# Performance work log

Measured on AMD Instinct MI355X. Metric: run time of the kernel, lower is better.

## Reference

```python
import jax, jax.numpy as jnp
import numpy as np

N = 50000          # num nodes
DEG = 16           # constant out-degree -> edges[:,0] sorted, every node present
E = N * DEG
NODE_IN = 128
NODE_OUT = 64
EDGE_IN = 128
EDGE_OUT = 64      # must equal NODE_OUT for the reshape in the original module


def _xavier_uniform(key, shape):
    fan_in, fan_out = shape[0], shape[1]
    a = np.sqrt(6.0 / (fan_in + fan_out)).astype(np.float32)
    return jax.random.uniform(key, shape, jnp.float32, -a, a)


def setup_inputs() -> dict:
    key = jax.random.key(0)
    k1, k2, k3, k4, k5, k6, k7 = jax.random.split(key, 7)
    node_fts = jax.random.normal(k1, (N, NODE_IN), jnp.float32)
    edge_fts = jax.random.normal(k2, (N, EDGE_IN), jnp.float32)
    # sorted sources with constant degree so unique(src).shape[0] == N and
    # the original's repeat(bincount) trick is equivalent to gather-by-src
    src = jnp.repeat(jnp.arange(N, dtype=jnp.int32), DEG)
    dst = jax.random.randint(k3, (E,), 0, N, dtype=jnp.int32)
    edges = jnp.stack([src, dst], axis=1)  # [E, 2]
    W_node = _xavier_uniform(k4, (NODE_IN, NODE_OUT))
    W_edge = _xavier_uniform(k5, (EDGE_IN, EDGE_OUT))
    a_node = _xavier_uniform(k6, (2 * NODE_OUT, 1))
    a_edge = _xavier_uniform(k7, (NODE_OUT + EDGE_OUT, 1))
    return {"node_fts": node_fts, "edge_fts": edge_fts, "edges": edges,
            "W_node": W_node, "W_edge": W_edge,
            "a_node": a_node, "a_edge": a_edge}


def reference(node_fts, edge_fts, edges, W_node, W_edge, a_node, a_edge):
    src = edges[:, 0]
    h_v = node_fts @ W_node            # [N, NODE_OUT]
    e_v = edge_fts @ W_edge            # [N, EDGE_OUT]

    # gather endpoint features -> [E, 2*NODE_OUT] / [E, NODE_OUT+EDGE_OUT]
    h_pair = h_v[edges].reshape(-1, 2 * NODE_OUT)
    e_pair = e_v[edges].reshape(-1, NODE_OUT + EDGE_OUT)

    leaky = lambda x: jnp.where(x > 0, x, 0.2 * x)
    node_att = leaky((h_pair @ a_node)[:, 0])   # [E]
    edge_att = leaky((e_pair @ a_edge)[:, 0])   # [E]

    node_att = jnp.exp(jnp.clip(node_att, -2.0, 2.0))
    edge_att = jnp.exp(jnp.clip(edge_att, -2.0, 2.0))

    node_sum = jax.ops.segment_sum(node_att, src, num_segments=N)
    edge_sum = jax.ops.segment_sum(edge_att, src, num_segments=N)

    node_att_norm = node_att / node_sum[src]
    edge_att_norm = edge_att / edge_sum[src]

    node_att_var = jnp.var(node_att_norm, ddof=1)  # torch.var is unbiased
    edge_att_var = jnp.var(edge_att_norm, ddof=1)

    node_out = jax.ops.segment_sum(h_pair * node_att_norm[:, None], src, num_segments=N)
    edge_out = jax.ops.segment_sum(e_pair * edge_att_norm[:, None], src, num_segments=N)
    return node_out, edge_out, node_att_var, edge_att_var
```

## Files before the change

### kernel.cpp

```cpp
#include <hip/hip_runtime.h>
#include <hip/hip_bf16.h>

#define NN 50000
#define DEG 16
#define EE (NN*DEG)
#define CHUNKS 3125

typedef unsigned int uint;
typedef unsigned short ushort;
typedef __attribute__((ext_vector_type(8))) short bf16x8;
typedef __attribute__((ext_vector_type(4))) float f32x4;

__device__ inline ushort f2b(float f){
  return __bfloat16_as_ushort(__float2bfloat16(f));
}
__device__ inline float b2f(uint lo16){ return __uint_as_float(lo16 << 16); }
__device__ inline float bhi(uint v){ return __uint_as_float(v & 0xffff0000u); }

__global__ __launch_bounds__(256) void prep_kernel(
    const float* __restrict__ W0, const float* __restrict__ W1,
    uint4* __restrict__ wf)
{
  const int pass = blockIdx.y;
  const float* W = pass ? W1 : W0;
  const int t    = threadIdx.x;
  const int f    = blockIdx.x*4 + (t >> 6);
  const int lane = t & 63;
  const int kt = f >> 2, nt = f & 3;
  const int n  = nt*16 + (lane & 15);
  const int k0 = kt*32 + (lane >> 4)*8;
  uint4 pk;
  ushort* ps = (ushort*)&pk;
  #pragma unroll
  for (int j = 0; j < 8; j++) ps[j] = f2b(W[(k0 + j)*64 + n]);
  wf[(pass*16 + f)*64 + lane] = pk;
}

__global__ __launch_bounds__(256) void gemm_mfma_kernel(
    const float* __restrict__ in0, const float* __restrict__ in1,
    const uint4* __restrict__ wf,
    const float* __restrict__ a0,  const float* __restrict__ a1,
    ushort* __restrict__ hev,
    float* __restrict__ s1ne, float* __restrict__ s2ne)
{
  const int pass = blockIdx.y;
  const float* in = pass ? in1 : in0;
  const float* av = pass ? a1  : a0;

  const int tid  = threadIdx.x;
  const int wv   = tid >> 6;
  const int lane = tid & 63;
  const int g    = lane >> 4;
  const int c    = lane & 15;

  const int ch = blockIdx.x*4 + wv;
  if (ch >= CHUNKS) return;
  const int r0 = ch * 16;

  bf16x8 wfrag[16];
  const uint4* wfp = wf + (long)pass*16*64 + lane;
  #pragma unroll
  for (int f = 0; f < 16; f++) {
    uint4 v = wfp[f*64];
    wfrag[f] = *(bf16x8*)&v;
  }
  float a1r[4][4], a2r[4][4];
  #pragma unroll
  for (int nt = 0; nt < 4; nt++)
    #pragma unroll
    for (int v = 0; v < 4; v++) {
      a1r[nt][v] = av[nt*16 + g*4 + v];
      a2r[nt][v] = av[64 + nt*16 + g*4 + v];
    }

  const float* rowp = in + (long)(r0 + c)*128 + g*8;
  float4 ald[8];
  #pragma unroll
  for (int kt = 0; kt < 4; kt++) {
    ald[kt*2]   = *(const float4*)(rowp + kt*32);
    ald[kt*2+1] = *(const float4*)(rowp + kt*32 + 4);
  }

  f32x4 acc[4];
  #pragma unroll
  for (int nt = 0; nt < 4; nt++) acc[nt] = (f32x4){0.f, 0.f, 0.f, 0.f};
  #pragma unroll
  for (int kt = 0; kt < 4; kt++) {
    const float4 u = ald[kt*2], w = ald[kt*2+1];
    bf16x8 af;
    af[0] = (short)f2b(u.x); af[1] = (short)f2b(u.y);
    af[2] = (short)f2b(u.z); af[3] = (short)f2b(u.w);
    af[4] = (short)f2b(w.x); af[5] = (short)f2b(w.y);
    af[6] = (short)f2b(w.z); af[7] = (short)f2b(w.w);
    #pragma unroll
    for (int nt = 0; nt < 4; nt++)
      acc[nt] = __builtin_amdgcn_mfma_f32_16x16x32_bf16(wfrag[kt*4+nt], af, acc[nt], 0, 0, 0);
  }

  float t1 = 0.f, t2 = 0.f;
  #pragma unroll
  for (int nt = 0; nt < 4; nt++)
    #pragma unroll
    for (int v = 0; v < 4; v++) {
      t1 = fmaf(acc[nt][v], a1r[nt][v], t1);
      t2 = fmaf(acc[nt][v], a2r[nt][v], t2);
    }
  t1 += __shfl_xor(t1, 16); t1 += __shfl_xor(t1, 32);
  t2 += __shfl_xor(t2, 16); t2 += __shfl_xor(t2, 32);
  if (lane < 16) {
    s1ne[(long)(r0 + lane)*2 + pass] = t1;
    s2ne[(long)(r0 + lane)*2 + pass] = t2;
  }

  ushort* rowt = hev + (long)(r0 + c)*128 + pass*64 + g*4;
  #pragma unroll
  for (int nt = 0; nt < 4; nt++) {
    uint2 pkv;
    pkv.x = (uint)f2b(acc[nt][0]) | ((uint)f2b(acc[nt][1]) << 16);
    pkv.y = (uint)f2b(acc[nt][2]) | ((uint)f2b(acc[nt][3]) << 16);
    *(uint2*)(rowt + nt*16) = pkv;
  }
}

__global__ __launch_bounds__(256) void attn_kernel(
    const uint* __restrict__ hev,
    const float2* __restrict__ s1ne, const float2* __restrict__ s2ne,
    const int* __restrict__ edges,
    float* __restrict__ outp, double* __restrict__ partials)
{
  const int tid  = threadIdx.x;
  const int wv   = tid >> 6;
  const int lane = tid & 63;
  const int j    = lane >> 4;
  const int cl   = lane & 15;
  double a_qn = 0.0, a_qe = 0.0;
  float* node_out = outp;
  float* edge_out = outp + (long)NN*128;
  const int NG = NN/4;

#define LOADT(dest, T) { \
    _Pragma("unroll") \
    for (int m = 0; m < 4; m++) { \
      const int sl = (T)*16 + m*4 + j; \
      const int d  = __shfl(dst, sl); \
      dest[m] = *(const uint4*)(hev + (long)d*64 + cl*4); \
    } }

#define COMB(T, src) { \
    float ac[8]; \
    _Pragma("unroll") for (int u = 0; u < 8; u++) ac[u] = 0.f; \
    _Pragma("unroll") \
    for (int m = 0; m < 4; m++) { \
      const int sl = (T)*16 + m*4 + j; \
      const float w2n = __shfl(wn, sl); \
      const float w2e = __shfl(we, sl); \
      const float wk  = (cl < 8) ? w2n : w2e; \
      const uint4 v = src[m]; \
      ac[0] = fmaf(wk, b2f(v.x & 0xffffu), ac[0]); \
      ac[1] = fmaf(wk, bhi(v.x),           ac[1]); \
      ac[2] = fmaf(wk, b2f(v.y & 0xffffu), ac[2]); \
      ac[3] = fmaf(wk, bhi(v.y),           ac[3]); \
      ac[4] = fmaf(wk, b2f(v.z & 0xffffu), ac[4]); \
      ac[5] = fmaf(wk, bhi(v.z),           ac[5]); \
      ac[6] = fmaf(wk, b2f(v.w & 0xffffu), ac[6]); \
      ac[7] = fmaf(wk, bhi(v.w),           ac[7]); \
    } \
    _Pragma("unroll") \
    for (int u = 0; u < 8; u++) { \
      ac[u] += __shfl_xor(ac[u], 16); \
      ac[u] += __shfl_xor(ac[u], 32); \
    } \
    if (lane < 16) { \
      float* base = ((cl < 8) ? node_out : edge_out) \
                    + (long)(i0 + (T))*128 + 64 + 8*(cl & 7); \
      *(float4*)(base)     = make_float4(ac[0], ac[1], ac[2], ac[3]); \
      *(float4*)(base + 4) = make_float4(ac[4], ac[5], ac[6], ac[7]); \
    } }

  for (int grp = blockIdx.x*4 + wv; grp < NG; grp += gridDim.x*4) {
    const int i0 = grp*4;
    const int dst = edges[((long)i0*16 + lane)*2 + 1];
    const float2 s1v = s1ne[i0 + j];
    const float2 gsc = s2ne[dst];
    float xn = s1v.x + gsc.x;
    float xe = s1v.y + gsc.y;
    xn = xn > 0.f ? xn : 0.2f*xn;
    xe = xe > 0.f ? xe : 0.2f*xe;
    xn = fminf(fmaxf(xn, -2.f), 2.f);
    xe = fminf(fmaxf(xe, -2.f), 2.f);
    const float an = expf(xn);
    const float ae = expf(xe);
    float sn = an, se = ae;
    #pragma unroll
    for (int off = 1; off < 16; off <<= 1) {
      sn += __shfl_xor(sn, off);
      se += __shfl_xor(se, off);
    }
    const float wn = an / sn;
    const float we = ae / se;

    uint4 g0[4], g1[4];
    LOADT(g0, 0);
    LOADT(g1, 1);

    {
      const uint4 ov = *(const uint4*)(hev + (long)(i0 + j)*64 + cl*4);
      float* ob = ((cl < 8) ? node_out : edge_out) + (long)(i0 + j)*128 + 8*(cl & 7);
      *(float4*)(ob)     = make_float4(b2f(ov.x & 0xffffu), bhi(ov.x),
                                       b2f(ov.y & 0xffffu), bhi(ov.y));
      *(float4*)(ob + 4) = make_float4(b2f(ov.z & 0xffffu), bhi(ov.z),
                                       b2f(ov.w & 0xffffu), bhi(ov.w));
    }
    float rq = wn*wn, re = we*we;
    #pragma unroll
    for (int off = 1; off < 64; off <<= 1) {
      rq += __shfl_xor(rq, off);
      re += __shfl_xor(re, off);
    }
    if (lane == 0) { a_qn += (double)rq; a_qe += (double)re; }

    COMB(0, g0);
    LOADT(g0, 2);
    COMB(1, g1);
    LOADT(g1, 3);
    COMB(2, g0);
    COMB(3, g1);
  }
#undef LOADT
#undef COMB

  __shared__ double red[4][2];
  if (lane == 0) { red[wv][0] = a_qn; red[wv][1] = a_qe; }
  __syncthreads();
  if (tid == 0) {
    double t0 = 0, t1 = 0;
    #pragma unroll
    for (int w = 0; w < 4; w++) { t0 += red[w][0]; t1 += red[w][1]; }
    double* p = partials + (long)blockIdx.x*2;
    p[0] = t0; p[1] = t1;
  }
}

__global__ __launch_bounds__(256) void finalize_kernel(
    const double* __restrict__ partials, int nparts, float* __restrict__ outp)
{
  const int tid = threadIdx.x;
  double l0 = 0, l1 = 0;
  for (int b = tid; b < nparts; b += 256) {
    l0 += partials[b*2+0]; l1 += partials[b*2+1];
  }
  __shared__ double red[256][2];
  red[tid][0] = l0; red[tid][1] = l1;
  __syncthreads();
  for (int s = 128; s > 0; s >>= 1) {
    if (tid < s) {
      red[tid][0] += red[tid+s][0];
      red[tid][1] += red[tid+s][1];
    }
    __syncthreads();
  }
  if (tid == 0) {
    const double E = (double)EE;
    const double S = (double)NN;
    double varn = (red[0][0] - S*S/E) / (E - 1.0);
    double vare = (red[0][1] - S*S/E) / (E - 1.0);
    outp[(long)NN*256 + 0] = (float)varn;
    outp[(long)NN*256 + 1] = (float)vare;
  }
}

extern "C" void kernel_launch(void* const* d_in, const int* in_sizes, int n_in,
                              void* d_out, int out_size, void* d_ws, size_t ws_size,
                              hipStream_t stream)
{
  const float* node_fts = (const float*)d_in[0];
  const float* edge_fts = (const float*)d_in[1];
  const int*   edges    = (const int*)d_in[2];
  const float* W_node   = (const float*)d_in[3];
  const float* W_edge   = (const float*)d_in[4];
  const float* a_node   = (const float*)d_in[5];
  const float* a_edge   = (const float*)d_in[6];

  char* ws = (char*)d_ws;
  ushort* hev = (ushort*)(ws);
  float* s1ne = (float*)(ws + 12800000);
  float* s2ne = (float*)(ws + 13200000);
  double* partials = (double*)(ws + 13600000);
  uint4* wf = (uint4*)(ws + 14000000);
  float* outp = (float*)d_out;

  hipLaunchKernelGGL(prep_kernel, dim3(4, 2), dim3(256), 0, stream,
                     W_node, W_edge, wf);
  hipLaunchKernelGGL(gemm_mfma_kernel, dim3(782, 2), dim3(256), 0, stream,
                     node_fts, edge_fts, wf, a_node, a_edge,
                     hev, s1ne, s2ne);
  const int AB = 3125;
  hipLaunchKernelGGL(attn_kernel, dim3(AB), dim3(256), 0, stream,
                     (const uint*)hev,
                     (const float2*)s1ne, (const float2*)s2ne,
                     edges, outp, partials);
  hipLaunchKernelGGL(finalize_kernel, dim3(1), dim3(256), 0, stream,
                     partials, AB, outp);
}
```

Baseline: 66.52 us.

## Stage GEMM output through LDS for coalesced stores and split scores into separate kernel

The GEMM kernel now has each wave process two 16-row chunks, with both chunks' inputs loaded up front. Results are staged through a shared-memory tile so that hev is written with full 16-byte coalesced stores instead of scattered 8-byte stores. The attention-score dot products leave the GEMM epilogue and move into a new score_kernel, which rereads the bf16 hev rows and computes the scores from those bf16-rounded values. This adds a kernel launch and a 12.8 MB reread of hev, and the scores now come from rounded values rather than fp32 accumulators.

```diff
diff --git a/kernel.cpp b/kernel.cpp
--- a/kernel.cpp
+++ b/kernel.cpp
@@ -39,13 +39,10 @@
 __global__ __launch_bounds__(256) void gemm_mfma_kernel(
     const float* __restrict__ in0, const float* __restrict__ in1,
     const uint4* __restrict__ wf,
-    const float* __restrict__ a0,  const float* __restrict__ a1,
-    ushort* __restrict__ hev,
-    float* __restrict__ s1ne, float* __restrict__ s2ne)
+    ushort* __restrict__ hev)
 {
   const int pass = blockIdx.y;
   const float* in = pass ? in1 : in0;
-  const float* av = pass ? a1  : a0;
 
   const int tid  = threadIdx.x;
   const int wv   = tid >> 6;
@@ -53,9 +50,13 @@
   const int g    = lane >> 4;
   const int c    = lane & 15;
 
-  const int ch = blockIdx.x*4 + wv;
-  if (ch >= CHUNKS) return;
-  const int r0 = ch * 16;
+  __shared__ ushort tile[4][16][72];
+
+  const int w   = blockIdx.x*4 + wv;
+  const int chA = w*2;
+  const int chB = chA + 1;
+  if (chA >= CHUNKS) return;
+  const bool hasB = (chB < CHUNKS);
 
   bf16x8 wfrag[16];
   const uint4* wfp = wf + (long)pass*16*64 + lane;
@@ -64,62 +65,112 @@
     uint4 v = wfp[f*64];
     wfrag[f] = *(bf16x8*)&v;
   }
-  float a1r[4][4], a2r[4][4];
+
+  float4 aldA[8], aldB[8];
+  {
+    const float* rowA = in + (long)(chA*16 + c)*128 + g*8;
+    #pragma unroll
+    for (int kt = 0; kt < 4; kt++) {
+      aldA[kt*2]   = *(const float4*)(rowA + kt*32);
+      aldA[kt*2+1] = *(const float4*)(rowA + kt*32 + 4);
+    }
+  }
+  if (hasB) {
+    const float* rowB = in + (long)(chB*16 + c)*128 + g*8;
+    #pragma unroll
+    for (int kt = 0; kt < 4; kt++) {
+      aldB[kt*2]   = *(const float4*)(rowB + kt*32);
+      aldB[kt*2+1] = *(const float4*)(rowB + kt*32 + 4);
+    }
+  }
+
+#define COMPUTE_STORE(ald, ch) { \
+    f32x4 acc[4]; \
+    _Pragma("unroll") \
+    for (int nt = 0; nt < 4; nt++) acc[nt] = (f32x4){0.f, 0.f, 0.f, 0.f}; \
+    _Pragma("unroll") \
+    for (int kt = 0; kt < 4; kt++) { \
+      const float4 u = ald[kt*2], x = ald[kt*2+1]; \
+      bf16x8 af; \
+      af[0] = (short)f2b(u.x); af[1] = (short)f2b(u.y); \
+      af[2] = (short)f2b(u.z); af[3] = (short)f2b(u.w); \
+      af[4] = (short)f2b(x.x); af[5] = (short)f2b(x.y); \
+      af[6] = (short)f2b(x.z); af[7] = (short)f2b(x.w); \
+      _Pragma("unroll") \
+      for (int nt = 0; nt < 4; nt++) \
+        acc[nt] = __builtin_amdgcn_mfma_f32_16x16x32_bf16(wfrag[kt*4+nt], af, acc[nt], 0, 0, 0); \
+    } \
+     \
+    ushort* tp = &tile[wv][c][g*4]; \
+    _Pragma("unroll") \
+    for (int nt = 0; nt < 4; nt++) { \
+      uint2 pkv; \
+      pkv.x = (uint)f2b(acc[nt][0]) | ((uint)f2b(acc[nt][1]) << 16); \
+      pkv.y = (uint)f2b(acc[nt][2]) | ((uint)f2b(acc[nt][3]) << 16); \
+      *(uint2*)(tp + nt*16) = pkv; \
+    } \
+     \
+    _Pragma("unroll") \
+    for (int q = 0; q < 2; q++) { \
+      const int idx = q*64 + lane; \
+      const int row = idx >> 3, col = idx & 7; \
+      uint4 val = *(const uint4*)&tile[wv][row][col*8]; \
+      *(uint4*)(hev + (long)((ch)*16 + row)*128 + pass*64 + col*8) = val; \
+    } \
+  }
+
+  COMPUTE_STORE(aldA, chA);
+  if (hasB) COMPUTE_STORE(aldB, chB);
+#undef COMPUTE_STORE
+}
+
+__global__ __launch_bounds__(256) void score_kernel(
+    const uint* __restrict__ hev,
+    const float* __restrict__ a0, const float* __restrict__ a1,
+    float* __restrict__ s1ne, float* __restrict__ s2ne)
+{
+  const long r = (long)blockIdx.x*256 + threadIdx.x;
+  if (r >= NN) return;
+  const uint* row = hev + r*64;
+  float s1n = 0.f, s2n = 0.f, s1e = 0.f, s2e = 0.f;
   #pragma unroll
-  for (int nt = 0; nt < 4; nt++)
-    #pragma unroll
-    for (int v = 0; v < 4; v++) {
-      a1r[nt][v] = av[nt*16 + g*4 + v];
-      a2r[nt][v] = av[64 + nt*16 + g*4 + v];
-    }
-
-  const float* rowp = in + (long)(r0 + c)*128 + g*8;
-  float4 ald[8];
+  for (int i = 0; i < 8; i++) {
+    const uint4 v = *(const uint4*)(row + i*4);
+    const float f0 = b2f(v.x & 0xffffu), f1 = bhi(v.x);
+    const float f2 = b2f(v.y & 0xffffu), f3 = bhi(v.y);
+    const float f4 = b2f(v.z & 0xffffu), f5 = bhi(v.z);
+    const float f6 = b2f(v.w & 0xffffu), f7 = bhi(v.w);
+    const float* p1 = a0 + i*8;
+    const float* p2 = a0 + 64 + i*8;
+    s1n = fmaf(f0,p1[0],s1n); s1n = fmaf(f1,p1[1],s1n);
+    s1n = fmaf(f2,p1[2],s1n); s1n = fmaf(f3,p1[3],s1n);
+    s1n = fmaf(f4,p1[4],s1n); s1n = fmaf(f5,p1[5],s1n);
+    s1n = fmaf(f6,p1[6],s1n); s1n = fmaf(f7,p1[7],s1n);
+    s2n = fmaf(f0,p2[0],s2n); s2n = fmaf(f1,p2[1],s2n);
+    s2n = fmaf(f2,p2[2],s2n); s2n = fmaf(f3,p2[3],s2n);
+    s2n = fmaf(f4,p2[4],s2n); s2n = fmaf(f5,p2[5],s2n);
+    s2n = fmaf(f6,p2[6],s2n); s2n = fmaf(f7,p2[7],s2n);
+  }
   #pragma unroll
-  for (int kt = 0; kt < 4; kt++) {
-    ald[kt*2]   = *(const float4*)(rowp + kt*32);
-    ald[kt*2+1] = *(const float4*)(rowp + kt*32 + 4);
-  }
-
-  f32x4 acc[4];
-  #pragma unroll
-  for (int nt = 0; nt < 4; nt++) acc[nt] = (f32x4){0.f, 0.f, 0.f, 0.f};
-  #pragma unroll
-  for (int kt = 0; kt < 4; kt++) {
-    const float4 u = ald[kt*2], w = ald[kt*2+1];
-    bf16x8 af;
-    af[0] = (short)f2b(u.x); af[1] = (short)f2b(u.y);
-    af[2] = (short)f2b(u.z); af[3] = (short)f2b(u.w);
-    af[4] = (short)f2b(w.x); af[5] = (short)f2b(w.y);
-    af[6] = (short)f2b(w.z); af[7] = (short)f2b(w.w);
-    #pragma unroll
-    for (int nt = 0; nt < 4; nt++)
-      acc[nt] = __builtin_amdgcn_mfma_f32_16x16x32_bf16(wfrag[kt*4+nt], af, acc[nt], 0, 0, 0);
-  }
-
-  float t1 = 0.f, t2 = 0.f;
-  #pragma unroll
-  for (int nt = 0; nt < 4; nt++)
-    #pragma unroll
-    for (int v = 0; v < 4; v++) {
-      t1 = fmaf(acc[nt][v], a1r[nt][v], t1);
-      t2 = fmaf(acc[nt][v], a2r[nt][v], t2);
-    }
-  t1 += __shfl_xor(t1, 16); t1 += __shfl_xor(t1, 32);
-  t2 += __shfl_xor(t2, 16); t2 += __shfl_xor(t2, 32);
-  if (lane < 16) {
-    s1ne[(long)(r0 + lane)*2 + pass] = t1;
-    s2ne[(long)(r0 + lane)*2 + pass] = t2;
-  }
-
-  ushort* rowt = hev + (long)(r0 + c)*128 + pass*64 + g*4;
-  #pragma unroll
-  for (int nt = 0; nt < 4; nt++) {
-    uint2 pkv;
-    pkv.x = (uint)f2b(acc[nt][0]) | ((uint)f2b(acc[nt][1]) << 16);
-    pkv.y = (uint)f2b(acc[nt][2]) | ((uint)f2b(acc[nt][3]) << 16);
-    *(uint2*)(rowt + nt*16) = pkv;
-  }
+  for (int i = 0; i < 8; i++) {
+    const uint4 v = *(const uint4*)(row + 32 + i*4);
+    const float f0 = b2f(v.x & 0xffffu), f1 = bhi(v.x);
+    const float f2 = b2f(v.y & 0xffffu), f3 = bhi(v.y);
+    const float f4 = b2f(v.z & 0xffffu), f5 = bhi(v.z);
+    const float f6 = b2f(v.w & 0xffffu), f7 = bhi(v.w);
+    const float* p1 = a1 + i*8;
+    const float* p2 = a1 + 64 + i*8;
+    s1e = fmaf(f0,p1[0],s1e); s1e = fmaf(f1,p1[1],s1e);
+    s1e = fmaf(f2,p1[2],s1e); s1e = fmaf(f3,p1[3],s1e);
+    s1e = fmaf(f4,p1[4],s1e); s1e = fmaf(f5,p1[5],s1e);
+    s1e = fmaf(f6,p1[6],s1e); s1e = fmaf(f7,p1[7],s1e);
+    s2e = fmaf(f0,p2[0],s2e); s2e = fmaf(f1,p2[1],s2e);
+    s2e = fmaf(f2,p2[2],s2e); s2e = fmaf(f3,p2[3],s2e);
+    s2e = fmaf(f4,p2[4],s2e); s2e = fmaf(f5,p2[5],s2e);
+    s2e = fmaf(f6,p2[6],s2e); s2e = fmaf(f7,p2[7],s2e);
+  }
+  s1ne[r*2+0] = s1n; s1ne[r*2+1] = s1e;
+  s2ne[r*2+0] = s2n; s2ne[r*2+1] = s2e;
 }
 
 __global__ __launch_bounds__(256) void attn_kernel(
@@ -291,9 +342,10 @@
 
   hipLaunchKernelGGL(prep_kernel, dim3(4, 2), dim3(256), 0, stream,
                      W_node, W_edge, wf);
-  hipLaunchKernelGGL(gemm_mfma_kernel, dim3(782, 2), dim3(256), 0, stream,
-                     node_fts, edge_fts, wf, a_node, a_edge,
-                     hev, s1ne, s2ne);
+  hipLaunchKernelGGL(gemm_mfma_kernel, dim3(391, 2), dim3(256), 0, stream,
+                     node_fts, edge_fts, wf, hev);
+  hipLaunchKernelGGL(score_kernel, dim3(196), dim3(256), 0, stream,
+                     (const uint*)hev, a_node, a_edge, s1ne, s2ne);
   const int AB = 3125;
   hipLaunchKernelGGL(attn_kernel, dim3(AB), dim3(256), 0, stream,
                      (const uint*)hev,
```

Measured after the change: 68.44 us. +2.9%, slower.
